# Kernel tuning notes

Measured on AMD Instinct MI355X. Metric: run time of the kernel, lower is better.

Reference implementation:

```python
import jax, jax.numpy as jnp
import numpy as np

N = 100000      # nodes
E = 3200000     # edges
F_IN = 128
HID = 64
NUM_CLASSES = 10
NUM_GRAPHS = 256


def setup_inputs() -> dict:
    key = jax.random.key(0)
    ks = jax.random.split(key, 12)
    x = jax.random.normal(ks[0], (N, F_IN), dtype=jnp.float32)
    edge_index = jax.random.randint(ks[1], (2, E), 0, N, dtype=jnp.int64)
    batch = jnp.sort(jax.random.randint(ks[2], (N,), 0, NUM_GRAPHS, dtype=jnp.int64))
    s = 1.0 / np.sqrt(F_IN)
    W1 = jax.random.uniform(ks[3], (F_IN, HID), jnp.float32, -s, s)
    b1 = jnp.zeros((HID,), jnp.float32)
    s2 = 1.0 / np.sqrt(HID)
    W2 = jax.random.uniform(ks[4], (HID, HID), jnp.float32, -s2, s2)
    b2 = jnp.zeros((HID,), jnp.float32)
    W3 = jax.random.uniform(ks[5], (HID, HID), jnp.float32, -s2, s2)
    b3 = jnp.zeros((HID,), jnp.float32)
    Wc = jax.random.uniform(ks[6], (HID, NUM_CLASSES), jnp.float32, -s2, s2)
    bc = jax.random.uniform(ks[7], (NUM_CLASSES,), jnp.float32, -s2, s2)
    return {"x": x, "edge_index": edge_index, "batch": batch,
            "W1": W1, "b1": b1, "W2": W2, "b2": b2, "W3": W3, "b3": b3,
            "Wc": Wc, "bc": bc}


def _gcn_norm(edge_index, num_nodes):
    # add self-loops, compute symmetric normalization D^-1/2 A_hat D^-1/2
    loop = jnp.arange(num_nodes, dtype=edge_index.dtype)
    src = jnp.concatenate([edge_index[0], loop])
    dst = jnp.concatenate([edge_index[1], loop])
    deg = jax.ops.segment_sum(jnp.ones_like(dst, dtype=jnp.float32), dst,
                              num_segments=num_nodes)
    dinv = jax.lax.rsqrt(deg)  # deg >= 1 due to self-loops
    norm = dinv[src] * dinv[dst]  # [E+N]
    return src, dst, norm


def _gcn_layer(x, W, b, src, dst, norm, num_nodes):
    h = x @ W                              # [N, H] dense transform first (PyG order)
    msg = norm[:, None] * h[src]           # gather + scale
    agg = jax.ops.segment_sum(msg, dst, num_segments=num_nodes)  # scatter-add
    return agg + b


def reference(x, edge_index, batch, W1, b1, W2, b2, W3, b3, Wc, bc):
    num_nodes = x.shape[0]
    src, dst, norm = _gcn_norm(edge_index, num_nodes)
    h = jax.nn.relu(_gcn_layer(x, W1, b1, src, dst, norm, num_nodes))
    h = jax.nn.relu(_gcn_layer(h, W2, b2, src, dst, norm, num_nodes))
    h = jax.nn.relu(_gcn_layer(h, W3, b3, src, dst, norm, num_nodes))
    # global mean pool over graphs
    sums = jax.ops.segment_sum(h, batch, num_segments=NUM_GRAPHS)
    cnt = jax.ops.segment_sum(jnp.ones((num_nodes,), jnp.float32), batch,
                              num_segments=NUM_GRAPHS)
    pooled = sums / jnp.maximum(cnt, 1.0)[:, None]   # [G, HID]
    return pooled @ Wc + bc                          # [G, NUM_CLASSES]
```

## Files before the change

### kernel.cpp

```cpp
#include <hip/hip_runtime.h>


#define NSUB 512
#define MAXNODES 256

typedef __attribute__((ext_vector_type(8))) short bf16x8;
typedef __attribute__((ext_vector_type(4))) float f32x4;

__device__ __forceinline__ unsigned short f2bf(float x) {
  unsigned u = __float_as_uint(x);
  u += 0x7FFFu + ((u >> 16) & 1u);
  return (unsigned short)(u >> 16);
}
__device__ __forceinline__ float bf2f(unsigned short h) {
  return __uint_as_float((unsigned)h << 16);
}
__device__ __forceinline__ float uf(unsigned u) { return __uint_as_float(u); }

__global__ void k_detect(const unsigned* __restrict__ ei, int* __restrict__ flag) {
  __shared__ int any;
  if (threadIdx.x == 0) any = 0;
  __syncthreads();
  unsigned v = 0;
  for (int i = threadIdx.x; i < 8192; i += blockDim.x) v |= ei[2 * i + 1];
  if (v) atomicOr(&any, 1);
  __syncthreads();
  if (threadIdx.x == 0) *flag = (any == 0) ? 1 : 0;
}

__device__ __forceinline__ int idx32(const int* p, long long i, bool wide) {
  return __builtin_nontemporal_load(p + (wide ? 2 * i : i));
}

__global__ __launch_bounds__(1024) void k_part(const void* __restrict__ eiv, int E,
                                               const int* __restrict__ flag, int cap2,
                                               int* __restrict__ scur,
                                               unsigned* __restrict__ ebuf2, int N) {
  __shared__ int cnt[NSUB];
  __shared__ int base[NSUB];
  __shared__ int off[NSUB];
  const int* ei = (const int*)eiv;
  const bool wide = (*flag != 0);
  const int tid = threadIdx.x;
  const int chunk = (E + gridDim.x - 1) / gridDim.x;
  const int c0 = blockIdx.x * chunk;
  const int c1 = (c0 + chunk < E) ? c0 + chunk : E;
  for (int i = tid; i < NSUB; i += 1024) { cnt[i] = 0; off[i] = 0; }
  __syncthreads();
  for (int e = c0 + tid; e < c1; e += 1024) {
    const int d = idx32(ei, (long long)E + e, wide);
    const int b = (int)(((long long)d * NSUB) / N);
    atomicAdd(&cnt[b], 1);
  }
  __syncthreads();
  for (int i = tid; i < NSUB; i += 1024) base[i] = atomicAdd(&scur[i], cnt[i]);
  __syncthreads();
  const long long cap = (long long)NSUB * cap2;
  for (int e = c0 + tid; e < c1; e += 1024) {
    const int d = idx32(ei, (long long)E + e, wide);
    const int s = idx32(ei, e, wide);
    const int b = (int)(((long long)d * NSUB) / N);
    const int nlo = (int)(((long long)N * b + NSUB - 1) / NSUB);
    const int o = atomicAdd(&off[b], 1);
    long long pos = (long long)b * cap2 + base[b] + o;
    if (pos >= cap) pos = cap - 1;
    ebuf2[pos] = ((unsigned)(d - nlo) << 24) | (unsigned)s;
  }
}

__global__ void k_sscan(const int* __restrict__ scur, int* __restrict__ sbase) {
  __shared__ int p[256];
  const int t = threadIdx.x;
  const int s0 = scur[2 * t], s1 = scur[2 * t + 1];
  const int v = s0 + s1;
  p[t] = v;
  __syncthreads();
  for (int off = 1; off < 256; off <<= 1) {
    const int tv = (t >= off) ? p[t - off] : 0;
    __syncthreads();
    p[t] += tv;
    __syncthreads();
  }
  const int excl = p[t] - v;
  sbase[2 * t] = excl;
  sbase[2 * t + 1] = excl + s0;
  if (t == 255) sbase[NSUB] = p[t];
}

__global__ __launch_bounds__(512) void k_build(const unsigned* __restrict__ ebuf2,
                                               const int* __restrict__ scur, int cap2,
                                               const int* __restrict__ sbase,
                                               int* __restrict__ rowptr,
                                               float* __restrict__ dinv,
                                               int* __restrict__ csr, int N) {
  __shared__ int hist[256];
  __shared__ int pref[256];
  const int s = blockIdx.x;
  const int t = threadIdx.x;
  int nlo = (int)(((long long)N * s + NSUB - 1) / NSUB);
  int nhi = (int)(((long long)N * (s + 1) + NSUB - 1) / NSUB);
  if (nhi > N) nhi = N;
  const int nn = nhi - nlo;
  if (t < 256) hist[t] = 0;
  __syncthreads();
  const long long e0 = (long long)s * cap2;
  const long long e1 = e0 + scur[s];
  for (long long e = e0 + t; e < e1; e += 512) {
    const unsigned v = __builtin_nontemporal_load(&ebuf2[e]);
    atomicAdd(&hist[v >> 24], 1);
  }
  __syncthreads();
  int h = 0;
  if (t < 256) {
    h = hist[t];
    pref[t] = h;
  }
  __syncthreads();
  for (int off = 1; off < 256; off <<= 1) {
    int tv = 0;
    if (t < 256 && t >= off) tv = pref[t - off];
    __syncthreads();
    if (t < 256) pref[t] += tv;
    __syncthreads();
  }
  if (t < 256) {
    const int cur0 = sbase[s] + pref[t] - h;
    if (t < nn) {
      rowptr[nlo + t] = cur0;
      dinv[nlo + t] = rsqrtf((float)(h + 1));
    }
    hist[t] = cur0;
  }
  if (s == NSUB - 1 && t == 0) rowptr[N] = sbase[NSUB];
  __syncthreads();
  for (long long e = e0 + t; e < e1; e += 512) {
    const unsigned v = ebuf2[e];
    const int pos = atomicAdd(&hist[v >> 24], 1);
    csr[pos] = (int)(v & 0x00FFFFFFu);
  }
}

template <int K, bool BF16IN>
__global__ __launch_bounds__(256) void k_gemm_mfma(const void* __restrict__ Xv,
                                                   const float* __restrict__ Wg,
                                                   const float* __restrict__ dinv,
                                                   unsigned short* __restrict__ HS,
                                                   int N) {
  __shared__ short Xl[64 * K];
  __shared__ short Wt[64 * K];
  const int t = threadIdx.x;
  const long long r0 = (long long)blockIdx.x * 64;
  const int rows = (int)((N - r0) < 64 ? (N - r0) : 64);

  for (int idx = t; idx < K * 64; idx += 256) {
    const int k = idx >> 6, n = idx & 63;
    Wt[n * K + (((k >> 3) ^ (n & 7)) << 3) + (k & 7)] = (short)f2bf(Wg[idx]);
  }
  const int CH = K / 8;
#pragma unroll
  for (int p = 0; p < K / 32; ++p) {
    const int c = p * 256 + t;
    const int row = c / CH, ch = c % CH;
    const int src = (row < rows) ? row : 0;
    bf16x8 h;
    if constexpr (BF16IN) {
      h = *(const bf16x8*)&((const unsigned short*)Xv)[(r0 + src) * K + ch * 8];
    } else {
      const float* X = (const float*)Xv;
      const float4 v0 = *(const float4*)&X[(r0 + src) * K + ch * 8];
      const float4 v1 = *(const float4*)&X[(r0 + src) * K + ch * 8 + 4];
      h[0] = (short)f2bf(v0.x); h[1] = (short)f2bf(v0.y);
      h[2] = (short)f2bf(v0.z); h[3] = (short)f2bf(v0.w);
      h[4] = (short)f2bf(v1.x); h[5] = (short)f2bf(v1.y);
      h[6] = (short)f2bf(v1.z); h[7] = (short)f2bf(v1.w);
    }
    *(bf16x8*)&Xl[row * K + ((ch ^ (row & 7)) << 3)] = h;
  }
  __syncthreads();

  const int lane = t & 63, w = t >> 6;
  const int lo = lane & 15, hi = lane >> 4;
  const int rowa = w * 16 + lo;

  f32x4 acc[4];
#pragma unroll
  for (int i = 0; i < 4; ++i) acc[i] = (f32x4){0.f, 0.f, 0.f, 0.f};

  bf16x8 a[K / 32];
#pragma unroll
  for (int kk = 0; kk < K / 32; ++kk)
    a[kk] = *(const bf16x8*)&Xl[rowa * K + (((kk * 4 + hi) ^ (rowa & 7)) << 3)];

#pragma unroll
  for (int n0 = 0; n0 < 4; ++n0) {
    const int n = n0 * 16 + lo;
#pragma unroll
    for (int kk = 0; kk < K / 32; ++kk) {
      const bf16x8 b = *(const bf16x8*)&Wt[n * K + (((kk * 4 + hi) ^ (n & 7)) << 3)];
      acc[n0] = __builtin_amdgcn_mfma_f32_16x16x32_bf16(a[kk], b, acc[n0], 0, 0, 0);
    }
  }

  float dv[4];
#pragma unroll
  for (int r = 0; r < 4; ++r) {
    const int rr = w * 16 + hi * 4 + r;
    dv[r] = dinv[r0 + (rr < rows ? rr : 0)];
  }
#pragma unroll
  for (int n0 = 0; n0 < 4; ++n0) {
#pragma unroll
    for (int r = 0; r < 4; ++r) {
      const int rr = w * 16 + hi * 4 + r;
      if (rr < rows)
        HS[(r0 + rr) * 64 + n0 * 16 + lo] = f2bf(dv[r] * acc[n0][r]);
    }
  }
}

__global__ void k_agg(const unsigned short* __restrict__ HS, const int* __restrict__ rowptr,
                      const int* __restrict__ csr, const float* __restrict__ dinv,
                      const float* __restrict__ bias, unsigned* __restrict__ OUT, int N) {
  const int lane = threadIdx.x & 63;
  const int wid = threadIdx.x >> 6;
  const int wpb = blockDim.x >> 6;
  const int c4 = lane & 15;
  const int q = lane >> 4;
  const float b0 = bias[4 * c4 + 0], b1 = bias[4 * c4 + 1];
  const float b2 = bias[4 * c4 + 2], b3 = bias[4 * c4 + 3];
  const uint2* __restrict__ H8 = (const uint2*)HS;
  uint2* __restrict__ O8 = (uint2*)OUT;
  const unsigned M = 0xffff0000u;
  for (int node = blockIdx.x * wpb + wid; node < N; node += wpb * gridDim.x) {
    const int s0 = rowptr[node], s1 = rowptr[node + 1];
    float a0 = 0.f, a1 = 0.f, a2 = 0.f, a3 = 0.f;
    float c0 = 0.f, c1 = 0.f, c2 = 0.f, c3 = 0.f;
    if (q == 0) {
      const uint2 u = H8[(long long)node * 16 + c4];
      a0 += uf(u.x << 16); a1 += uf(u.x & M);
      a2 += uf(u.y << 16); a3 += uf(u.y & M);
    }
    for (int base = s0; base < s1; base += 64) {
      int m = s1 - base;
      if (m > 64) m = 64;
      const int idx = (base + lane < s1) ? csr[base + lane] : 0;
      const int ng = m >> 2;
      int g = 0;
      for (; g + 2 <= ng; g += 2) {
        const int e0 = __shfl(idx, 4 * g + q, 64);
        const int e1 = __shfl(idx, 4 * g + 4 + q, 64);
        const uint2 u0 = H8[(long long)e0 * 16 + c4];
        const uint2 u1 = H8[(long long)e1 * 16 + c4];
        a0 += uf(u0.x << 16); a1 += uf(u0.x & M);
        a2 += uf(u0.y << 16); a3 += uf(u0.y & M);
        c0 += uf(u1.x << 16); c1 += uf(u1.x & M);
        c2 += uf(u1.y << 16); c3 += uf(u1.y & M);
      }
      for (; g < ng; ++g) {
        const int e0 = __shfl(idx, 4 * g + q, 64);
        const uint2 u0 = H8[(long long)e0 * 16 + c4];
        a0 += uf(u0.x << 16); a1 += uf(u0.x & M);
        a2 += uf(u0.y << 16); a3 += uf(u0.y & M);
      }
      const int r = m & 3;
      if (r) {
        const int e = __shfl(idx, (m & ~3) + (q < r ? q : 0), 64);
        if (q < r) {
          const uint2 u = H8[(long long)e * 16 + c4];
          a0 += uf(u.x << 16); a1 += uf(u.x & M);
          a2 += uf(u.y << 16); a3 += uf(u.y & M);
        }
      }
    }
    a0 += c0; a1 += c1; a2 += c2; a3 += c3;
    a0 += __shfl_xor(a0, 16, 64); a0 += __shfl_xor(a0, 32, 64);
    a1 += __shfl_xor(a1, 16, 64); a1 += __shfl_xor(a1, 32, 64);
    a2 += __shfl_xor(a2, 16, 64); a2 += __shfl_xor(a2, 32, 64);
    a3 += __shfl_xor(a3, 16, 64); a3 += __shfl_xor(a3, 32, 64);
    if (q == 0) {
      const float dv = dinv[node];
      const unsigned short o0 = f2bf(fmaxf(fmaf(dv, a0, b0), 0.f));
      const unsigned short o1 = f2bf(fmaxf(fmaf(dv, a1, b1), 0.f));
      const unsigned short o2 = f2bf(fmaxf(fmaf(dv, a2, b2), 0.f));
      const unsigned short o3 = f2bf(fmaxf(fmaf(dv, a3, b3), 0.f));
      uint2 o;
      o.x = (unsigned)o0 | ((unsigned)o1 << 16);
      o.y = (unsigned)o2 | ((unsigned)o3 << 16);
      O8[(long long)node * 16 + c4] = o;
    }
  }
}

__global__ void k_pool(const unsigned short* __restrict__ H, const void* __restrict__ batch,
                       const int* __restrict__ flag, float* __restrict__ pooled, int N) {
  __shared__ int se[2];
  __shared__ float red[4][64];
  bool wide = (*flag != 0);
  int g = blockIdx.x;
  if (threadIdx.x < 2) {
    int target = g + threadIdx.x;
    int lo = 0, hi = N;
    while (lo < hi) {
      int mid = (lo + hi) >> 1;
      long long v = wide ? ((const long long*)batch)[mid] : (long long)((const int*)batch)[mid];
      if (v < target) lo = mid + 1; else hi = mid;
    }
    se[threadIdx.x] = lo;
  }
  __syncthreads();
  int s = se[0], e = se[1];
  int lane = threadIdx.x & 63, wid = threadIdx.x >> 6;
  float acc = 0.f;
  for (int r = s + wid; r < e; r += 4) acc += bf2f(H[(long long)r * 64 + lane]);
  red[wid][lane] = acc;
  __syncthreads();
  if (wid == 0) {
    float v = red[0][lane] + red[1][lane] + red[2][lane] + red[3][lane];
    float cnt = (float)(e - s);
    pooled[g * 64 + lane] = v / fmaxf(cnt, 1.f);
  }
}

__global__ void k_classify(const float* __restrict__ pooled, const float* __restrict__ Wc,
                           const float* __restrict__ bc, float* __restrict__ out, int total) {
  int t = blockIdx.x * blockDim.x + threadIdx.x;
  if (t >= total) return;
  int g = t / 10, c = t % 10;
  float acc = bc[c];
#pragma unroll
  for (int h = 0; h < 64; ++h) acc += pooled[g * 64 + h] * Wc[h * 10 + c];
  out[t] = acc;
}

extern "C" void kernel_launch(void* const* d_in, const int* in_sizes, int n_in,
                              void* d_out, int out_size, void* d_ws, size_t ws_size,
                              hipStream_t stream) {
  const float* x = (const float*)d_in[0];
  const void* ei = d_in[1];
  const void* batch = d_in[2];
  const float* W1 = (const float*)d_in[3];
  const float* b1 = (const float*)d_in[4];
  const float* W2 = (const float*)d_in[5];
  const float* b2 = (const float*)d_in[6];
  const float* W3 = (const float*)d_in[7];
  const float* b3 = (const float*)d_in[8];
  const float* Wc = (const float*)d_in[9];
  const float* bc = (const float*)d_in[10];
  float* out = (float*)d_out;

  const int N = in_sizes[0] / 128;
  const int E = in_sizes[1] / 2;
  const int G = out_size / 10;
  const int cap2 = E / NSUB + E / NSUB / 8 + 64;

  char* W = (char*)d_ws;
  size_t off = 0;
  auto take = [&](size_t b) -> void* {
    void* p = W + off;
    off += (b + 255) & ~(size_t)255;
    return p;
  };
  int* flag = (int*)take(4);
  int* rowptr = (int*)take((size_t)4 * (N + 1));
  int* scur = (int*)take((size_t)4 * NSUB);
  int* sbase = (int*)take((size_t)4 * (NSUB + 1));
  float* dinv = (float*)take((size_t)4 * N);
  int* csr = (int*)take((size_t)4 * E);
  unsigned short* hs = (unsigned short*)take((size_t)2 * N * 64);
  unsigned short* cur = (unsigned short*)take((size_t)2 * N * 64);
  unsigned* ebuf2 = (unsigned*)take((size_t)4 * NSUB * cap2);
  float* pooled = (float*)take((size_t)4 * G * 64);
  (void)ws_size;

  hipMemsetAsync(scur, 0, (size_t)4 * NSUB, stream);

  k_detect<<<1, 256, 0, stream>>>((const unsigned*)ei, flag);
  k_part<<<512, 1024, 0, stream>>>(ei, E, flag, cap2, scur, ebuf2, N);
  k_sscan<<<1, 256, 0, stream>>>(scur, sbase);
  k_build<<<NSUB, 512, 0, stream>>>(ebuf2, scur, cap2, sbase, rowptr, dinv, csr, N);

  const int TILES = (N + 63) / 64;
  k_gemm_mfma<128, false><<<TILES, 256, 0, stream>>>(x, W1, dinv, hs, N);
  k_agg<<<4096, 256, 0, stream>>>(hs, rowptr, csr, dinv, b1, (unsigned*)cur, N);
  k_gemm_mfma<64, true><<<TILES, 256, 0, stream>>>(cur, W2, dinv, hs, N);
  k_agg<<<4096, 256, 0, stream>>>(hs, rowptr, csr, dinv, b2, (unsigned*)cur, N);
  k_gemm_mfma<64, true><<<TILES, 256, 0, stream>>>(cur, W3, dinv, hs, N);
  k_agg<<<4096, 256, 0, stream>>>(hs, rowptr, csr, dinv, b3, (unsigned*)cur, N);

  k_pool<<<G, 256, 0, stream>>>(cur, batch, flag, pooled, N);
  k_classify<<<(G * 10 + 255) / 256, 256, 0, stream>>>(pooled, Wc, bc, out, G * 10);
}
```

Before: 344.0 us.

## Fuse aggregation with next-layer GEMM and merge small setup/tail kernels

Aggregation for layers 1 and 2 is fused with the next layer's MFMA GEMM in one kernel per 64-node tile. The relu'd aggregated rows are staged in LDS instead of being written to global and read back. The index-width detection moves into the partition kernel, the segment scan is recomputed redundantly in each build block, and pooling is merged with the classifier, which cuts the number of launches. The fused kernel gives each wave 16 nodes in sequence across only TILES blocks, which may hurt load balance and latency hiding for the irregular gathers compared with the old grid-stride aggregation.

```diff
diff --git a/kernel.cpp b/kernel.cpp
--- a/kernel.cpp
+++ b/kernel.cpp
@@ -17,36 +17,33 @@
 }
 __device__ __forceinline__ float uf(unsigned u) { return __uint_as_float(u); }
 
-__global__ void k_detect(const unsigned* __restrict__ ei, int* __restrict__ flag) {
-  __shared__ int any;
-  if (threadIdx.x == 0) any = 0;
-  __syncthreads();
-  unsigned v = 0;
-  for (int i = threadIdx.x; i < 8192; i += blockDim.x) v |= ei[2 * i + 1];
-  if (v) atomicOr(&any, 1);
-  __syncthreads();
-  if (threadIdx.x == 0) *flag = (any == 0) ? 1 : 0;
-}
-
 __device__ __forceinline__ int idx32(const int* p, long long i, bool wide) {
   return __builtin_nontemporal_load(p + (wide ? 2 * i : i));
 }
 
 __global__ __launch_bounds__(1024) void k_part(const void* __restrict__ eiv, int E,
-                                               const int* __restrict__ flag, int cap2,
+                                               int* __restrict__ flag, int cap2,
                                                int* __restrict__ scur,
                                                unsigned* __restrict__ ebuf2, int N) {
   __shared__ int cnt[NSUB];
   __shared__ int base[NSUB];
   __shared__ int off[NSUB];
+  __shared__ int s_any;
+  const unsigned* eu = (const unsigned*)eiv;
   const int* ei = (const int*)eiv;
-  const bool wide = (*flag != 0);
   const int tid = threadIdx.x;
+  if (tid == 0) s_any = 0;
+  __syncthreads();
+  unsigned vv = 0;
+  for (int i = tid; i < 8192; i += 1024) vv |= eu[2 * i + 1];
+  if (vv) atomicOr(&s_any, 1);
+  for (int i = tid; i < NSUB; i += 1024) { cnt[i] = 0; off[i] = 0; }
+  __syncthreads();
+  const bool wide = (s_any == 0);
+  if (blockIdx.x == 0 && tid == 0) *flag = wide ? 1 : 0;
   const int chunk = (E + gridDim.x - 1) / gridDim.x;
   const int c0 = blockIdx.x * chunk;
   const int c1 = (c0 + chunk < E) ? c0 + chunk : E;
-  for (int i = tid; i < NSUB; i += 1024) { cnt[i] = 0; off[i] = 0; }
-  __syncthreads();
   for (int e = c0 + tid; e < c1; e += 1024) {
     const int d = idx32(ei, (long long)E + e, wide);
     const int b = (int)(((long long)d * NSUB) / N);
@@ -68,35 +65,28 @@
   }
 }
 
-__global__ void k_sscan(const int* __restrict__ scur, int* __restrict__ sbase) {
-  __shared__ int p[256];
-  const int t = threadIdx.x;
-  const int s0 = scur[2 * t], s1 = scur[2 * t + 1];
-  const int v = s0 + s1;
-  p[t] = v;
-  __syncthreads();
-  for (int off = 1; off < 256; off <<= 1) {
-    const int tv = (t >= off) ? p[t - off] : 0;
-    __syncthreads();
-    p[t] += tv;
-    __syncthreads();
-  }
-  const int excl = p[t] - v;
-  sbase[2 * t] = excl;
-  sbase[2 * t + 1] = excl + s0;
-  if (t == 255) sbase[NSUB] = p[t];
-}
-
 __global__ __launch_bounds__(512) void k_build(const unsigned* __restrict__ ebuf2,
                                                const int* __restrict__ scur, int cap2,
-                                               const int* __restrict__ sbase,
                                                int* __restrict__ rowptr,
                                                float* __restrict__ dinv,
                                                int* __restrict__ csr, int N) {
+  __shared__ int sc[NSUB];
   __shared__ int hist[256];
   __shared__ int pref[256];
   const int s = blockIdx.x;
   const int t = threadIdx.x;
+  if (t < NSUB) sc[t] = scur[t];
+  __syncthreads();
+  for (int off = 1; off < NSUB; off <<= 1) {
+    int tv = 0;
+    if (t < NSUB && t >= off) tv = sc[t - off];
+    __syncthreads();
+    if (t < NSUB) sc[t] += tv;
+    __syncthreads();
+  }
+  const int mycnt = scur[s];
+  const int sb = sc[s] - mycnt;
+  const int total = sc[NSUB - 1];
   int nlo = (int)(((long long)N * s + NSUB - 1) / NSUB);
   int nhi = (int)(((long long)N * (s + 1) + NSUB - 1) / NSUB);
   if (nhi > N) nhi = N;
@@ -104,7 +94,7 @@
   if (t < 256) hist[t] = 0;
   __syncthreads();
   const long long e0 = (long long)s * cap2;
-  const long long e1 = e0 + scur[s];
+  const long long e1 = e0 + mycnt;
   for (long long e = e0 + t; e < e1; e += 512) {
     const unsigned v = __builtin_nontemporal_load(&ebuf2[e]);
     atomicAdd(&hist[v >> 24], 1);
@@ -124,14 +114,14 @@
     __syncthreads();
   }
   if (t < 256) {
-    const int cur0 = sbase[s] + pref[t] - h;
+    const int cur0 = sb + pref[t] - h;
     if (t < nn) {
       rowptr[nlo + t] = cur0;
       dinv[nlo + t] = rsqrtf((float)(h + 1));
     }
     hist[t] = cur0;
   }
-  if (s == NSUB - 1 && t == 0) rowptr[N] = sbase[NSUB];
+  if (s == NSUB - 1 && t == 0) rowptr[N] = total;
   __syncthreads();
   for (long long e = e0 + t; e < e1; e += 512) {
     const unsigned v = ebuf2[e];
@@ -218,20 +208,37 @@
   }
 }
 
-__global__ void k_agg(const unsigned short* __restrict__ HS, const int* __restrict__ rowptr,
-                      const int* __restrict__ csr, const float* __restrict__ dinv,
-                      const float* __restrict__ bias, unsigned* __restrict__ OUT, int N) {
-  const int lane = threadIdx.x & 63;
-  const int wid = threadIdx.x >> 6;
-  const int wpb = blockDim.x >> 6;
+__global__ __launch_bounds__(256) void k_agg_gemm(
+    const unsigned short* __restrict__ HSin, const int* __restrict__ rowptr,
+    const int* __restrict__ csr, const float* __restrict__ dinv,
+    const float* __restrict__ bias, const float* __restrict__ Wg,
+    unsigned short* __restrict__ HSout, int N) {
+  __shared__ short Xl[64 * 64];
+  __shared__ short Wt[64 * 64];
+  const int t = threadIdx.x;
+  const long long r0 = (long long)blockIdx.x * 64;
+  const int rows = (int)((N - r0) < 64 ? (N - r0) : 64);
+  for (int idx = t; idx < 64 * 64; idx += 256) {
+    const int k = idx >> 6, n = idx & 63;
+    Wt[n * 64 + (((k >> 3) ^ (n & 7)) << 3) + (k & 7)] = (short)f2bf(Wg[idx]);
+  }
+  if (rows < 64) {
+    for (int i = t; i < 64 * 64; i += 256) Xl[i] = 0;
+  }
+  __syncthreads();
+
+  const int lane = t & 63;
+  const int wid = t >> 6;
   const int c4 = lane & 15;
   const int q = lane >> 4;
-  const float b0 = bias[4 * c4 + 0], b1 = bias[4 * c4 + 1];
-  const float b2 = bias[4 * c4 + 2], b3 = bias[4 * c4 + 3];
-  const uint2* __restrict__ H8 = (const uint2*)HS;
-  uint2* __restrict__ O8 = (uint2*)OUT;
+  const float bb0 = bias[4 * c4 + 0], bb1 = bias[4 * c4 + 1];
+  const float bb2 = bias[4 * c4 + 2], bb3 = bias[4 * c4 + 3];
+  const uint2* __restrict__ H8 = (const uint2*)HSin;
   const unsigned M = 0xffff0000u;
-  for (int node = blockIdx.x * wpb + wid; node < N; node += wpb * gridDim.x) {
+  for (int i = 0; i < 16; ++i) {
+    const int row = wid * 16 + i;
+    if (row >= rows) break;
+    const int node = (int)(r0 + row);
     const int s0 = rowptr[node], s1 = rowptr[node + 1];
     float a0 = 0.f, a1 = 0.f, a2 = 0.f, a3 = 0.f;
     float c0 = 0.f, c1 = 0.f, c2 = 0.f, c3 = 0.f;
@@ -262,10 +269,119 @@
         a0 += uf(u0.x << 16); a1 += uf(u0.x & M);
         a2 += uf(u0.y << 16); a3 += uf(u0.y & M);
       }
-      const int r = m & 3;
-      if (r) {
-        const int e = __shfl(idx, (m & ~3) + (q < r ? q : 0), 64);
-        if (q < r) {
+      const int rm = m & 3;
+      if (rm) {
+        const int e = __shfl(idx, (m & ~3) + (q < rm ? q : 0), 64);
+        if (q < rm) {
+          const uint2 u = H8[(long long)e * 16 + c4];
+          a0 += uf(u.x << 16); a1 += uf(u.x & M);
+          a2 += uf(u.y << 16); a3 += uf(u.y & M);
+        }
+      }
+    }
+    a0 += c0; a1 += c1; a2 += c2; a3 += c3;
+    a0 += __shfl_xor(a0, 16, 64); a0 += __shfl_xor(a0, 32, 64);
+    a1 += __shfl_xor(a1, 16, 64); a1 += __shfl_xor(a1, 32, 64);
+    a2 += __shfl_xor(a2, 16, 64); a2 += __shfl_xor(a2, 32, 64);
+    a3 += __shfl_xor(a3, 16, 64); a3 += __shfl_xor(a3, 32, 64);
+    if (q == 0) {
+      const float dv = dinv[node];
+      const unsigned short o0 = f2bf(fmaxf(fmaf(dv, a0, bb0), 0.f));
+      const unsigned short o1 = f2bf(fmaxf(fmaf(dv, a1, bb1), 0.f));
+      const unsigned short o2 = f2bf(fmaxf(fmaf(dv, a2, bb2), 0.f));
+      const unsigned short o3 = f2bf(fmaxf(fmaf(dv, a3, bb3), 0.f));
+      uint2 o;
+      o.x = (unsigned)o0 | ((unsigned)o1 << 16);
+      o.y = (unsigned)o2 | ((unsigned)o3 << 16);
+      const int ch = c4 >> 1;
+      *(uint2*)&Xl[row * 64 + ((ch ^ (row & 7)) << 3) + (c4 & 1) * 4] = o;
+    }
+  }
+  __syncthreads();
+
+  const int lo = lane & 15, hi = lane >> 4;
+  const int rowa = wid * 16 + lo;
+  f32x4 acc[4];
+#pragma unroll
+  for (int i = 0; i < 4; ++i) acc[i] = (f32x4){0.f, 0.f, 0.f, 0.f};
+  bf16x8 a[2];
+#pragma unroll
+  for (int kk = 0; kk < 2; ++kk)
+    a[kk] = *(const bf16x8*)&Xl[rowa * 64 + (((kk * 4 + hi) ^ (rowa & 7)) << 3)];
+#pragma unroll
+  for (int n0 = 0; n0 < 4; ++n0) {
+    const int n = n0 * 16 + lo;
+#pragma unroll
+    for (int kk = 0; kk < 2; ++kk) {
+      const bf16x8 b = *(const bf16x8*)&Wt[n * 64 + (((kk * 4 + hi) ^ (n & 7)) << 3)];
+      acc[n0] = __builtin_amdgcn_mfma_f32_16x16x32_bf16(a[kk], b, acc[n0], 0, 0, 0);
+    }
+  }
+  float dvv[4];
+#pragma unroll
+  for (int r = 0; r < 4; ++r) {
+    const int rr = wid * 16 + hi * 4 + r;
+    dvv[r] = dinv[r0 + (rr < rows ? rr : 0)];
+  }
+#pragma unroll
+  for (int n0 = 0; n0 < 4; ++n0) {
+#pragma unroll
+    for (int r = 0; r < 4; ++r) {
+      const int rr = wid * 16 + hi * 4 + r;
+      if (rr < rows)
+        HSout[(r0 + rr) * 64 + n0 * 16 + lo] = f2bf(dvv[r] * acc[n0][r]);
+    }
+  }
+}
+
+__global__ void k_agg(const unsigned short* __restrict__ HS, const int* __restrict__ rowptr,
+                      const int* __restrict__ csr, const float* __restrict__ dinv,
+                      const float* __restrict__ bias, unsigned* __restrict__ OUT, int N) {
+  const int lane = threadIdx.x & 63;
+  const int wid = threadIdx.x >> 6;
+  const int wpb = blockDim.x >> 6;
+  const int c4 = lane & 15;
+  const int q = lane >> 4;
+  const float b0 = bias[4 * c4 + 0], b1 = bias[4 * c4 + 1];
+  const float b2 = bias[4 * c4 + 2], b3 = bias[4 * c4 + 3];
+  const uint2* __restrict__ H8 = (const uint2*)HS;
+  uint2* __restrict__ O8 = (uint2*)OUT;
+  const unsigned M = 0xffff0000u;
+  for (int node = blockIdx.x * wpb + wid; node < N; node += wpb * gridDim.x) {
+    const int s0 = rowptr[node], s1 = rowptr[node + 1];
+    float a0 = 0.f, a1 = 0.f, a2 = 0.f, a3 = 0.f;
+    float c0 = 0.f, c1 = 0.f, c2 = 0.f, c3 = 0.f;
+    if (q == 0) {
+      const uint2 u = H8[(long long)node * 16 + c4];
+      a0 += uf(u.x << 16); a1 += uf(u.x & M);
+      a2 += uf(u.y << 16); a3 += uf(u.y & M);
+    }
+    for (int base = s0; base < s1; base += 64) {
+      int m = s1 - base;
+      if (m > 64) m = 64;
+      const int idx = (base + lane < s1) ? csr[base + lane] : 0;
+      const int ng = m >> 2;
+      int g = 0;
+      for (; g + 2 <= ng; g += 2) {
+        const int e0 = __shfl(idx, 4 * g + q, 64);
+        const int e1 = __shfl(idx, 4 * g + 4 + q, 64);
+        const uint2 u0 = H8[(long long)e0 * 16 + c4];
+        const uint2 u1 = H8[(long long)e1 * 16 + c4];
+        a0 += uf(u0.x << 16); a1 += uf(u0.x & M);
+        a2 += uf(u0.y << 16); a3 += uf(u0.y & M);
+        c0 += uf(u1.x << 16); c1 += uf(u1.x & M);
+        c2 += uf(u1.y << 16); c3 += uf(u1.y & M);
+      }
+      for (; g < ng; ++g) {
+        const int e0 = __shfl(idx, 4 * g + q, 64);
+        const uint2 u0 = H8[(long long)e0 * 16 + c4];
+        a0 += uf(u0.x << 16); a1 += uf(u0.x & M);
+        a2 += uf(u0.y << 16); a3 += uf(u0.y & M);
+      }
+      const int rm = m & 3;
+      if (rm) {
+        const int e = __shfl(idx, (m & ~3) + (q < rm ? q : 0), 64);
+        if (q < rm) {
           const uint2 u = H8[(long long)e * 16 + c4];
           a0 += uf(u.x << 16); a1 += uf(u.x & M);
           a2 += uf(u.y << 16); a3 += uf(u.y & M);
@@ -291,10 +407,13 @@
   }
 }
 
-__global__ void k_pool(const unsigned short* __restrict__ H, const void* __restrict__ batch,
-                       const int* __restrict__ flag, float* __restrict__ pooled, int N) {
+__global__ void k_poolcls(const unsigned short* __restrict__ H,
+                          const void* __restrict__ batch, const int* __restrict__ flag,
+                          const float* __restrict__ Wc, const float* __restrict__ bc,
+                          float* __restrict__ out, int N) {
   __shared__ int se[2];
   __shared__ float red[4][64];
+  __shared__ float pl[64];
   bool wide = (*flag != 0);
   int g = blockIdx.x;
   if (threadIdx.x < 2) {
@@ -317,19 +436,15 @@
   if (wid == 0) {
     float v = red[0][lane] + red[1][lane] + red[2][lane] + red[3][lane];
     float cnt = (float)(e - s);
-    pooled[g * 64 + lane] = v / fmaxf(cnt, 1.f);
-  }
-}
-
-__global__ void k_classify(const float* __restrict__ pooled, const float* __restrict__ Wc,
-                           const float* __restrict__ bc, float* __restrict__ out, int total) {
-  int t = blockIdx.x * blockDim.x + threadIdx.x;
-  if (t >= total) return;
-  int g = t / 10, c = t % 10;
-  float acc = bc[c];
-#pragma unroll
-  for (int h = 0; h < 64; ++h) acc += pooled[g * 64 + h] * Wc[h * 10 + c];
-  out[t] = acc;
+    pl[lane] = v / fmaxf(cnt, 1.f);
+  }
+  __syncthreads();
+  if (threadIdx.x < 10) {
+    float a = bc[threadIdx.x];
+#pragma unroll
+    for (int h = 0; h < 64; ++h) a += pl[h] * Wc[h * 10 + threadIdx.x];
+    out[g * 10 + threadIdx.x] = a;
+  }
 }
 
 extern "C" void kernel_launch(void* const* d_in, const int* in_sizes, int n_in,
@@ -363,30 +478,23 @@
   int* flag = (int*)take(4);
   int* rowptr = (int*)take((size_t)4 * (N + 1));
   int* scur = (int*)take((size_t)4 * NSUB);
-  int* sbase = (int*)take((size_t)4 * (NSUB + 1));
   float* dinv = (float*)take((size_t)4 * N);
   int* csr = (int*)take((size_t)4 * E);
-  unsigned short* hs = (unsigned short*)take((size_t)2 * N * 64);
-  unsigned short* cur = (unsigned short*)take((size_t)2 * N * 64);
+  unsigned short* hsA = (unsigned short*)take((size_t)2 * N * 64);
+  unsigned short* hsB = (unsigned short*)take((size_t)2 * N * 64);
   unsigned* ebuf2 = (unsigned*)take((size_t)4 * NSUB * cap2);
-  float* pooled = (float*)take((size_t)4 * G * 64);
   (void)ws_size;
 
   hipMemsetAsync(scur, 0, (size_t)4 * NSUB, stream);
 
-  k_detect<<<1, 256, 0, stream>>>((const unsigned*)ei, flag);
   k_part<<<512, 1024, 0, stream>>>(ei, E, flag, cap2, scur, ebuf2, N);
-  k_sscan<<<1, 256, 0, stream>>>(scur, sbase);
-  k_build<<<NSUB, 512, 0, stream>>>(ebuf2, scur, cap2, sbase, rowptr, dinv, csr, N);
+  k_build<<<NSUB, 512, 0, stream>>>(ebuf2, scur, cap2, rowptr, dinv, csr, N);
 
   const int TILES = (N + 63) / 64;
-  k_gemm_mfma<128, false><<<TILES, 256, 0, stream>>>(x, W1, dinv, hs, N);
-  k_agg<<<4096, 256, 0, stream>>>(hs, rowptr, csr, dinv, b1, (unsigned*)cur, N);
-  k_gemm_mfma<64, true><<<TILES, 256, 0, stream>>>(cur, W2, dinv, hs, N);
-  k_agg<<<4096, 256, 0, stream>>>(hs, rowptr, csr, dinv, b2, (unsigned*)cur, N);
-  k_gemm_mfma<64, true><<<TILES, 256, 0, stream>>>(cur, W3, dinv, hs, N);
-  k_agg<<<4096, 256, 0, stream>>>(hs, rowptr, csr, dinv, b3, (unsigned*)cur, N);
-
-  k_pool<<<G, 256, 0, stream>>>(cur, batch, flag, pooled, N);
-  k_classify<<<(G * 10 + 255) / 256, 256, 0, stream>>>(pooled, Wc, bc, out, G * 10);
-}
+  k_gemm_mfma<128, false><<<TILES, 256, 0, stream>>>(x, W1, dinv, hsA, N);
+  k_agg_gemm<<<TILES, 256, 0, stream>>>(hsA, rowptr, csr, dinv, b1, W2, hsB, N);
+  k_agg_gemm<<<TILES, 256, 0, stream>>>(hsB, rowptr, csr, dinv, b2, W3, hsA, N);
+  k_agg<<<4096, 256, 0, stream>>>(hsA, rowptr, csr, dinv, b3, (unsigned*)hsB, N);
+
+  k_poolcls<<<G, 256, 0, stream>>>(hsB, batch, flag, Wc, bc, out, N);
+}
```

New measurement: 330.1 us. -4.0%, faster.
